# Kernel optimization log

Measured on AMD Instinct MI355X. Metric: run time of the kernel, lower is better.

The kernel has to match this reference:

```python
import jax, jax.numpy as jnp
import numpy as np

NH = 6
D = 78  # dim_k = dim_v, dk = dv = 13 per head
SCALE = 1.0 / np.sqrt(D // NH).astype(np.float32)


def _split(t):
    # (B, n, D) -> (B, H, n, dk)
    B, n, d = t.shape
    return t.reshape(B, n, NH, d // NH).transpose(0, 2, 1, 3)


def _merge(t):
    # (B, H, n, dk) -> (B, n, D)
    B, h, n, d = t.shape
    return t.transpose(0, 2, 1, 3).reshape(B, n, h * d)


def _cross_attn(x, y, Wq, Wk, Wv):
    # MultiHeadCrossSelfAttention / MultiHeadSelfAttention math (dropout=identity in eval;
    # attn_mask is expanded but never applied in the original forward).
    q = _split(x @ Wq)
    k = _split(y @ Wk)
    v = _split(y @ Wv)
    dist = jax.nn.softmax(jnp.einsum('bhqd,bhkd->bhqk', q, k) * SCALE, axis=-1)
    return _merge(jnp.einsum('bhqk,bhkd->bhqd', dist, v))


def _contrastive_attn(x, y, Wq, Wk, Wv):
    # MultiHeadContrastiveSelfAttention: softmax -> (1 - p) -> softmax -> matmul, residual q add.
    q = _split(x @ Wq)
    k = _split(y @ Wk)
    v = _split(y @ Wv)
    dist = jax.nn.softmax(jnp.einsum('bhqd,bhkd->bhqk', q, k) * SCALE, axis=-1)
    dist = jax.nn.softmax(1.0 - dist, axis=-1)
    return _merge(q + jnp.einsum('bhqk,bhkd->bhqd', dist, v))


def setup_inputs() -> dict:
    key = jax.random.key(0)
    ks = jax.random.split(key, 20)
    B, nT, nV, nA = 8, 1024, 1024, 1024
    inp = {
        'x': jax.random.normal(ks[0], (B, nT, D), jnp.float32),
        'y': jax.random.normal(ks[1], (B, nV, D), jnp.float32),
        'z': jax.random.normal(ks[2], (B, nA, D), jnp.float32),
        'mask_tv': jnp.zeros((B, nT, nV), jnp.bool_),
        'mask_ta': jnp.zeros((B, nT, nA), jnp.bool_),
    }
    names = ['Wq_tv', 'Wk_tv', 'Wv_tv', 'Wq_ta', 'Wk_ta', 'Wv_ta',
             'Wq_ctv', 'Wk_ctv', 'Wv_ctv', 'Wq_cta', 'Wk_cta', 'Wv_cta',
             'Wq_s', 'Wk_s', 'Wv_s']
    for i, nm in enumerate(names):
        inp[nm] = jax.random.normal(ks[3 + i], (D, D), jnp.float32) * 0.05
    return inp


def reference(x, y, z, mask_tv, mask_ta,
              Wq_tv, Wk_tv, Wv_tv, Wq_ta, Wk_ta, Wv_ta,
              Wq_ctv, Wk_ctv, Wv_ctv, Wq_cta, Wk_cta, Wv_cta,
              Wq_s, Wk_s, Wv_s):
    # masks are dead args in the original module (expanded but never applied)
    att_tv = _cross_attn(x, y, Wq_tv, Wk_tv, Wv_tv)          # MHSCA_TV
    att_ta = _cross_attn(x, z, Wq_ta, Wk_ta, Wv_ta)          # MHSCA_TA
    c_tv = _contrastive_attn(x, y, Wq_ctv, Wk_ctv, Wv_ctv)   # MHSCTA_TV
    c_ta = _contrastive_attn(x, z, Wq_cta, Wk_cta, Wv_cta)   # MHSCTA_TA
    # fuse three pooled modality tokens through the length-3 MHSA
    tokens = jnp.stack([x.mean(axis=1),
                        (att_tv + c_tv).mean(axis=1),
                        (att_ta + c_ta).mean(axis=1)], axis=1)  # (B, 3, D)
    fused = _cross_attn(tokens, tokens, Wq_s, Wk_s, Wv_s)       # MHSA
    # (B, 4*1024 + 3, D)
    return jnp.concatenate([att_tv, c_tv, att_ta, c_ta, fused], axis=1)
```

## Files before the change

kernel.cpp:

```cpp
#include <hip/hip_runtime.h>
#include <hip/hip_bf16.h>

#define BB 8
#define NN 1024
#define DM 78
#define NH 6
#define DK 13
#define NROW 4099
#define QSCL 0.40013158f
#define SCALE 0.27735009811261457f
#define INV1023 0.000977517106549365f

using bf16 = __hip_bfloat16;
typedef __attribute__((ext_vector_type(8))) short short8;
typedef __attribute__((ext_vector_type(4))) float f32x4;

#if __has_builtin(__builtin_amdgcn_exp2f)
#define EXP2(x) __builtin_amdgcn_exp2f(x)
#else
__device__ __forceinline__ float EXP2(float x) {
    float r;
    asm volatile("v_exp_f32 %0, %1\n\ts_nop 1" : "=v"(r) : "v"(x));
    return r;
}
#endif

#define MATSZ ((size_t)48 * 1024 * 16)

struct PW { const float* w[12]; };

__device__ __forceinline__ unsigned pkbf2(float a, float b) {
    __hip_bfloat162 t = __float22bfloat162_rn(make_float2(a, b));
    return *(unsigned*)&t;
}

union FRAG { unsigned u[4]; short8 s8; };

__global__ __launch_bounds__(256, 6) void proj_kernel(const float* __restrict__ x,
                                                      const float* __restrict__ y,
                                                      const float* __restrict__ z,
                                                      PW p,
                                                      unsigned* __restrict__ Qbf,
                                                      unsigned* __restrict__ Kbf,
                                                      unsigned* __restrict__ Vt,
                                                      float* __restrict__ Qf32,
                                                      float* __restrict__ sv,
                                                      float* __restrict__ tok) {
    __shared__ unsigned SMEM[6608];
    int bid = blockIdx.x;
    int tid = threadIdx.x;
    int mat, rb;
    if (bid < 256) { mat = 2 + (bid >> 7); rb = bid & 127; }
    else {
        int t = bid - 256;
        int midx = t >> 7;
        mat = (midx < 2) ? midx : midx + 2;
        rb = t & 127;
    }
    const float* src = (mat < 4) ? x : (((mat - 4) & 1) ? z : y);
    const float* sp = src + (size_t)rb * 64 * DM;
    const float* W = p.w[mat];
    int bb = rb >> 4;
    int i0 = (rb & 15) * 64;
    float* CT = (float*)SMEM;

    if (bid < 256) {
        float* AT = (float*)SMEM;
        float* WL = AT + 39 * 68;
        int rowg = tid >> 4, colg = tid & 15;
        float acc[4][5] = {{0.f}};
        for (int ch = 0; ch < 2; ++ch) {
            int e0 = ch * 39;
            if (ch) __syncthreads();
            for (int i = tid; i < 64 * 39; i += 256) {
                int r = i / 39, er = i - r * 39;
                AT[er * 68 + r] = sp[r * DM + e0 + er];
            }
            for (int i = tid; i < 39 * 80; i += 256) {
                int er = i / 80, c = i - er * 80;
                WL[er * 80 + c] = (c < DM) ? W[(size_t)(e0 + er) * DM + c] : 0.f;
            }
            __syncthreads();
            if (mat == 2 && tid < 39) {
                float s = 0.f;
                for (int r = 0; r < 64; ++r) s += AT[tid * 68 + r];
                atomicAdd(&tok[bb * DM + e0 + tid], s);
            }
            for (int er = 0; er < 39; ++er) {
                float4 a4 = *(const float4*)&AT[er * 68 + rowg * 4];
                float av[4] = {a4.x, a4.y, a4.z, a4.w};
                const float* wr = &WL[er * 80 + colg * 5];
                float w0 = wr[0], w1 = wr[1], w2 = wr[2], w3 = wr[3], w4 = wr[4];
#pragma unroll
                for (int j = 0; j < 4; ++j) {
                    acc[j][0] = fmaf(av[j], w0, acc[j][0]);
                    acc[j][1] = fmaf(av[j], w1, acc[j][1]);
                    acc[j][2] = fmaf(av[j], w2, acc[j][2]);
                    acc[j][3] = fmaf(av[j], w3, acc[j][3]);
                    acc[j][4] = fmaf(av[j], w4, acc[j][4]);
                }
            }
        }
        __syncthreads();
#pragma unroll
        for (int j = 0; j < 4; ++j)
#pragma unroll
            for (int k = 0; k < 5; ++k) {
                int c = colg * 5 + k;
                if (c < DM) CT[(rowg * 4 + j) * 81 + c] = acc[j][k];
            }
        __syncthreads();
        for (int t2 = tid; t2 < NH * 64 * 8; t2 += 256) {
            int hh = t2 >> 9;
            int rem = t2 & 511;
            int r = rem >> 3, cp = rem & 7;
            int c0 = cp * 2, c1 = cp * 2 + 1;
            float a = (c0 < DK) ? CT[r * 81 + hh * DK + c0] * QSCL : 0.f;
            float bv = (c1 < DK) ? CT[r * 81 + hh * DK + c1] * QSCL : 0.f;
            Qbf[(((size_t)mat * 48 + bb * NH + hh) * 1024 + i0 + r) * 8 + cp] = pkbf2(a, bv);
        }
        for (int t2 = tid; t2 < 64 * DM; t2 += 256) {
            int r = t2 / DM, c = t2 - r * DM;
            int hh = c / DK, dd = c - hh * DK;
            Qf32[((size_t)(mat - 2) * 48 + bb * NH + hh) * 1024 * DK +
                 (size_t)(i0 + r) * DK + dd] = CT[r * 81 + c];
        }
    } else {
        unsigned* ALu = SMEM;
        unsigned* WTu = SMEM + 64 * 52;
        const float2* sp2 = (const float2*)sp;
        for (int i = tid; i < 64 * 39; i += 256) {
            float2 f2 = sp2[i];
            int r = i / 39, pc = i - r * 39;
            ALu[r * 52 + pc] = pkbf2(f2.x, f2.y);
        }
        for (int i = tid; i < 64 * 13; i += 256) {
            int r = i / 13, pc = i - r * 13;
            ALu[r * 52 + 39 + pc] = 0u;
        }
        for (int i = tid; i < 41 * 80; i += 256) {
            int pc = i / 80, n = i - pc * 80;
            int k0 = pc * 2;
            float a = (n < DM && k0 < DM) ? W[(size_t)k0 * DM + n] : 0.f;
            float bv = (n < DM && k0 + 1 < DM) ? W[(size_t)(k0 + 1) * DM + n] : 0.f;
            WTu[n * 41 + pc] = pkbf2(a, bv);
        }
        __syncthreads();
        int wv = tid >> 6, lane = tid & 63, quad = lane >> 4, lq = lane & 15;
        int r0 = wv * 16;
        const short* ALs = (const short*)ALu;
        const short* WTs = (const short*)WTu;
        short8 af0 = *(const short8*)(ALs + (r0 + lq) * 104 + quad * 8);
        short8 af1 = *(const short8*)(ALs + (r0 + lq) * 104 + 32 + quad * 8);
        short8 af2 = *(const short8*)(ALs + (r0 + lq) * 104 + 64 + quad * 8);
        const f32x4 zz = {0.f, 0.f, 0.f, 0.f};
        f32x4 acc[5];
#pragma unroll
        for (int n = 0; n < 5; ++n) acc[n] = zz;
#pragma unroll
        for (int n = 0; n < 5; ++n) {
            const short* wb = WTs + (n * 16 + lq) * 82 + quad * 8;
            acc[n] = __builtin_amdgcn_mfma_f32_16x16x32_bf16(
                af0, *(const short8*)wb, acc[n], 0, 0, 0);
            acc[n] = __builtin_amdgcn_mfma_f32_16x16x32_bf16(
                af1, *(const short8*)(wb + 32), acc[n], 0, 0, 0);
            acc[n] = __builtin_amdgcn_mfma_f32_16x16x32_bf16(
                af2, *(const short8*)(wb + 64), acc[n], 0, 0, 0);
        }
        __syncthreads();
#pragma unroll
        for (int n = 0; n < 5; ++n) {
            int c = n * 16 + lq;
            if (c < DM) {
#pragma unroll
                for (int r = 0; r < 4; ++r)
                    CT[(r0 + quad * 4 + r) * 81 + c] = acc[n][r];
            }
        }
        __syncthreads();
        if (mat < 8) {
            unsigned* dst = (mat < 4) ? Qbf : Kbf;
            int m4 = (mat < 4) ? mat : mat - 4;
            float scl = (mat < 4) ? QSCL : 1.0f;
            for (int t2 = tid; t2 < NH * 64 * 8; t2 += 256) {
                int hh = t2 >> 9;
                int rem = t2 & 511;
                int r = rem >> 3, cp = rem & 7;
                int c0 = cp * 2, c1 = cp * 2 + 1;
                float a = (c0 < DK) ? CT[r * 81 + hh * DK + c0] * scl : 0.f;
                float bv = (c1 < DK) ? CT[r * 81 + hh * DK + c1] * scl : 0.f;
                dst[(((size_t)m4 * 48 + bb * NH + hh) * 1024 + i0 + r) * 8 + cp] = pkbf2(a, bv);
            }
        } else {
            for (int t2 = tid; t2 < NH * 16 * 32; t2 += 256) {
                int hh = t2 >> 9;
                int rem = t2 & 511;
                int dd = rem >> 5, cp = rem & 31;
                int pp = (cp & 15) * 2;
                int b2 = cp >> 4;
                int qd = pp >> 3, jj = pp & 7;
                int l0 = b2 * 32 + 4 * qd + (jj < 4 ? jj : 12 + jj);
                float a, bv;
                if (dd < DK) {
                    a = CT[l0 * 81 + hh * DK + dd];
                    bv = CT[(l0 + 1) * 81 + hh * DK + dd];
                } else if (dd == 13) { a = 1.f; bv = 1.f; }
                else { a = 0.f; bv = 0.f; }
                Vt[(((size_t)(mat - 8) * 48 + bb * NH + hh) * 16 + dd) * 512 +
                   (i0 >> 1) + cp] = pkbf2(a, bv);
            }
            if (mat >= 10 && tid < DM) {
                int hh = tid / DK, dd = tid - hh * DK;
                float s = 0.f;
                for (int r = 0; r < 64; ++r) s += CT[r * 81 + tid];
                atomicAdd(&sv[((size_t)(mat - 10) * 48 + bb * NH + hh) * DK + dd], s);
            }
        }
    }
}

__global__ __launch_bounds__(256) void att_kernel(const bf16* __restrict__ Qbf,
                                                  const bf16* __restrict__ Kbf,
                                                  const bf16* __restrict__ Vt,
                                                  const float* __restrict__ Qf32,
                                                  const float* __restrict__ sv,
                                                  float* __restrict__ tok,
                                                  float* __restrict__ out) {
    int bid = blockIdx.x;
    int qt = (bid >> 3) & 7;
    int ghb = (bid & 7) | ((bid >> 6) << 3);
    int h = ghb % NH;
    int r2 = ghb / NH;
    int b = r2 & 7;
    int g = r2 >> 3;
    int tid = threadIdx.x, wave = tid >> 6, lane = tid & 63;
    int quad = lane >> 4, lq = lane & 15;
    size_t mb = (size_t)g * 48 + b * NH + h;
    int q0 = qt * 64 + wave * 16;
    int q1 = q0 + 512;

    short8 zero8 = {0, 0, 0, 0, 0, 0, 0, 0};
    short8 qfA = zero8, qfB = zero8;
    if (quad < 2) {
        qfA = *(const short8*)((const short*)Qbf + (mb * 1024 + q0 + lq) * 16 + quad * 8);
        qfB = *(const short8*)((const short*)Qbf + (mb * 1024 + q1 + lq) * 16 + quad * 8);
    }
    const short* Kp = (const short*)Kbf + mb * 1024 * 16;
    const short* Vp = (const short*)Vt + mb * 16 * 1024 + (size_t)lq * 1024;
    f32x4 OA = {0.f, 0.f, 0.f, 0.f};
    f32x4 OB = {0.f, 0.f, 0.f, 0.f};
    const f32x4 zz = {0.f, 0.f, 0.f, 0.f};

    short8 kX0 = zero8, kX1 = zero8, kY0 = zero8, kY1 = zero8, vX, vY;
    if (quad < 2) {
        kX0 = *(const short8*)(Kp + lq * 16 + quad * 8);
        kX1 = *(const short8*)(Kp + (16 + lq) * 16 + quad * 8);
        kY0 = *(const short8*)(Kp + (32 + lq) * 16 + quad * 8);
        kY1 = *(const short8*)(Kp + (48 + lq) * 16 + quad * 8);
    }
    vX = *(const short8*)(Vp + quad * 8);
    vY = *(const short8*)(Vp + 32 + quad * 8);

    for (int kt = 0; kt < 16; ++kt) {
        int nkey = kt * 64 + 64;
        f32x4 SX0 = __builtin_amdgcn_mfma_f32_16x16x32_bf16(kX0, qfA, zz, 0, 0, 0);
        f32x4 SX1 = __builtin_amdgcn_mfma_f32_16x16x32_bf16(kX1, qfA, zz, 0, 0, 0);
        f32x4 SX2 = __builtin_amdgcn_mfma_f32_16x16x32_bf16(kX0, qfB, zz, 0, 0, 0);
        f32x4 SX3 = __builtin_amdgcn_mfma_f32_16x16x32_bf16(kX1, qfB, zz, 0, 0, 0);
        f32x4 SY0 = __builtin_amdgcn_mfma_f32_16x16x32_bf16(kY0, qfA, zz, 0, 0, 0);
        f32x4 SY1 = __builtin_amdgcn_mfma_f32_16x16x32_bf16(kY1, qfA, zz, 0, 0, 0);
        f32x4 SY2 = __builtin_amdgcn_mfma_f32_16x16x32_bf16(kY0, qfB, zz, 0, 0, 0);
        f32x4 SY3 = __builtin_amdgcn_mfma_f32_16x16x32_bf16(kY1, qfB, zz, 0, 0, 0);
        short8 kX0n = zero8, kX1n = zero8, kY0n = zero8, kY1n = zero8, vXn, vYn;
        if (quad < 2) {
            kX0n = *(const short8*)(Kp + (nkey + lq) * 16 + quad * 8);
            kX1n = *(const short8*)(Kp + (nkey + 16 + lq) * 16 + quad * 8);
            kY0n = *(const short8*)(Kp + (nkey + 32 + lq) * 16 + quad * 8);
            kY1n = *(const short8*)(Kp + (nkey + 48 + lq) * 16 + quad * 8);
        }
        vXn = *(const short8*)(Vp + nkey + quad * 8);
        vYn = *(const short8*)(Vp + nkey + 32 + quad * 8);

        FRAG aXA, aXB, aYA, aYB;
        aXA.u[0] = pkbf2(EXP2(SX0[0]), EXP2(SX0[1]));
        aXA.u[1] = pkbf2(EXP2(SX0[2]), EXP2(SX0[3]));
        aXA.u[2] = pkbf2(EXP2(SX1[0]), EXP2(SX1[1]));
        aXA.u[3] = pkbf2(EXP2(SX1[2]), EXP2(SX1[3]));
        OA = __builtin_amdgcn_mfma_f32_16x16x32_bf16(aXA.s8, vX, OA, 0, 0, 0);
        aXB.u[0] = pkbf2(EXP2(SX2[0]), EXP2(SX2[1]));
        aXB.u[1] = pkbf2(EXP2(SX2[2]), EXP2(SX2[3]));
        aXB.u[2] = pkbf2(EXP2(SX3[0]), EXP2(SX3[1]));
        aXB.u[3] = pkbf2(EXP2(SX3[2]), EXP2(SX3[3]));
        OB = __builtin_amdgcn_mfma_f32_16x16x32_bf16(aXB.s8, vX, OB, 0, 0, 0);
        aYA.u[0] = pkbf2(EXP2(SY0[0]), EXP2(SY0[1]));
        aYA.u[1] = pkbf2(EXP2(SY0[2]), EXP2(SY0[3]));
        aYA.u[2] = pkbf2(EXP2(SY1[0]), EXP2(SY1[1]));
        aYA.u[3] = pkbf2(EXP2(SY1[2]), EXP2(SY1[3]));
        OA = __builtin_amdgcn_mfma_f32_16x16x32_bf16(aYA.s8, vY, OA, 0, 0, 0);
        aYB.u[0] = pkbf2(EXP2(SY2[0]), EXP2(SY2[1]));
        aYB.u[1] = pkbf2(EXP2(SY2[2]), EXP2(SY2[3]));
        aYB.u[2] = pkbf2(EXP2(SY3[0]), EXP2(SY3[1]));
        aYB.u[3] = pkbf2(EXP2(SY3[2]), EXP2(SY3[3]));
        OB = __builtin_amdgcn_mfma_f32_16x16x32_bf16(aYB.s8, vY, OB, 0, 0, 0);
        kX0 = kX0n; kX1 = kX1n; kY0 = kY0n; kY1 = kY1n; vX = vXn; vY = vYn;
    }

    size_t rowbase = (g == 0) ? 0 : (g == 1 ? 2 * NN : (g == 2 ? NN : 3 * NN));
    float lA[4], lB[4];
#pragma unroll
    for (int r = 0; r < 4; ++r) {
        lA[r] = __shfl(OA[r], (lane & 48) | 13, 64);
        lB[r] = __shfl(OB[r], (lane & 48) | 13, 64);
    }
    float svv = 0.f;
    const float* qf32p = nullptr;
    if (g >= 2) {
        if (lq < DK) svv = sv[((size_t)(g - 2) * 48 + b * NH + h) * DK + lq];
        qf32p = Qf32 + ((size_t)(g - 2) * 48 + b * NH + h) * 1024 * DK + lq;
    }
    float vsum = 0.f;
#pragma unroll
    for (int r = 0; r < 4; ++r) {
        int mA = q0 + quad * 4 + r;
        int mB = q1 + quad * 4 + r;
        float A0 = OA[r] / lA[r];
        float A1 = OB[r] / lB[r];
        float v0, v1;
        if (g < 2) { v0 = A0; v1 = A1; }
        else {
            float qr0 = (lq < DK) ? qf32p[(size_t)mA * DK] : 0.f;
            float qr1 = (lq < DK) ? qf32p[(size_t)mB * DK] : 0.f;
            v0 = qr0 + (svv - A0) * INV1023;
            v1 = qr1 + (svv - A1) * INV1023;
        }
        if (lq < DK) {
            out[((size_t)b * NROW + rowbase + mA) * DM + h * DK + lq] = v0;
            out[((size_t)b * NROW + rowbase + mB) * DM + h * DK + lq] = v1;
            vsum += v0 + v1;
        }
    }
    vsum += __shfl_xor(vsum, 16);
    vsum += __shfl_xor(vsum, 32);
    if (quad == 0 && lq < DK) {
        int tki = (g & 1) ? 2 : 1;
        atomicAdd(&tok[(size_t)tki * (8 * DM) + b * DM + h * DK + lq], vsum);
    }
}

__global__ __launch_bounds__(256) void fused_kernel(const float* __restrict__ tok,
                                                    const float* __restrict__ Wq,
                                                    const float* __restrict__ Wk,
                                                    const float* __restrict__ Wv,
                                                    float* __restrict__ out) {
    __shared__ float T[3 * DM], Qs[3 * DM], Ks[3 * DM], Vs[3 * DM], P[NH * 9];
    int b = blockIdx.x, tid = threadIdx.x;
    if (tid < 234) {
        int t = tid / DM, d = tid - t * DM;
        T[tid] = tok[(size_t)t * (8 * DM) + b * DM + d] * (1.f / NN);
    }
    __syncthreads();
    for (int idx = tid; idx < 702; idx += 256) {
        int mat = idx / 234;
        int rem = idx - mat * 234;
        int t = rem / DM, d = rem - t * DM;
        const float* W = (mat == 0) ? Wq : (mat == 1 ? Wk : Wv);
        float a = 0.f;
        for (int e = 0; e < DM; ++e) a = fmaf(T[t * DM + e], W[(size_t)e * DM + d], a);
        float* dst = (mat == 0) ? Qs : (mat == 1 ? Ks : Vs);
        dst[t * DM + d] = a;
    }
    __syncthreads();
    if (tid < NH * 3) {
        int h = tid / 3, t = tid % 3;
        float s[3];
        for (int k = 0; k < 3; ++k) {
            float a = 0.f;
            for (int d2 = 0; d2 < DK; ++d2)
                a += Qs[t * DM + h * DK + d2] * Ks[k * DM + h * DK + d2];
            s[k] = a * SCALE;
        }
        float mm = fmaxf(s[0], fmaxf(s[1], s[2]));
        float e0 = __expf(s[0] - mm), e1 = __expf(s[1] - mm), e2 = __expf(s[2] - mm);
        float inv = 1.f / (e0 + e1 + e2);
        P[(h * 3 + t) * 3 + 0] = e0 * inv;
        P[(h * 3 + t) * 3 + 1] = e1 * inv;
        P[(h * 3 + t) * 3 + 2] = e2 * inv;
    }
    __syncthreads();
    if (tid < 234) {
        int t = tid / DM, d = tid - t * DM, h = d / DK;
        float a = 0.f;
        for (int k = 0; k < 3; ++k) a += P[(h * 3 + t) * 3 + k] * Vs[k * DM + d];
        out[((size_t)b * NROW + 4 * NN + t) * DM + d] = a;
    }
}

extern "C" void kernel_launch(void* const* d_in, const int* in_sizes, int n_in,
                              void* d_out, int out_size, void* d_ws, size_t ws_size,
                              hipStream_t stream) {
    const float* bigs[3] = {nullptr, nullptr, nullptr};
    const float* w[15];
    int nb = 0, nw = 0;
    for (int i = 0; i < n_in; ++i) {
        if (in_sizes[i] == BB * NN * DM && nb < 3) bigs[nb++] = (const float*)d_in[i];
        else if (in_sizes[i] == DM * DM && nw < 15) w[nw++] = (const float*)d_in[i];
    }
    if (nb < 3 || nw < 15) {
        bigs[0] = (const float*)d_in[0]; bigs[1] = (const float*)d_in[1];
        bigs[2] = (const float*)d_in[2];
        int base = (n_in >= 20) ? 5 : 3;
        for (int i = 0; i < 15; ++i) w[i] = (const float*)d_in[base + i];
    }
    const float* x = bigs[0];
    const float* y = bigs[1];
    const float* z = bigs[2];
    float* out = (float*)d_out;

    bf16* Qbf = (bf16*)d_ws;
    bf16* Kbf = Qbf + 4 * MATSZ;
    bf16* Vt  = Kbf + 4 * MATSZ;
    float* Qf32 = (float*)(Vt + 4 * MATSZ);
    float* sv = Qf32 + (size_t)2 * 48 * 1024 * DK;
    float* tok = sv + 2 * 48 * DK;

    PW pp;
    const float* wsel[12] = {w[0], w[3], w[6], w[9],
                             w[1], w[4], w[7], w[10],
                             w[2], w[5], w[8], w[11]};
    for (int i = 0; i < 12; ++i) pp.w[i] = wsel[i];

    hipMemsetAsync(sv, 0, (2 * 48 * DK + 3 * 8 * DM) * sizeof(float), stream);
    proj_kernel<<<1536, 256, 0, stream>>>(x, y, z, pp, (unsigned*)Qbf, (unsigned*)Kbf,
                                          (unsigned*)Vt, Qf32, sv, tok);
    att_kernel<<<4 * BB * NH * 8, 256, 0, stream>>>(Qbf, Kbf, Vt, Qf32, sv, tok, out);
    fused_kernel<<<BB, 256, 0, stream>>>(tok, w[12], w[13], w[14], out);
}
```

Measured before the change: 212.5 us.

## Unify projection onto MFMA path and use K=16 MFMA with deeper prefetch in attention

The projection kernel drops its scalar-FMA fp32 path for the x-based Q matrices and runs all matrices through the bf16 MFMA path, computing token sums from the bf16-packed tile. The attention loop replaces the zero-padded 16x16x32 score MFMAs with 16x16x16 MFMAs on 4-element K/Q fragments, which halves wasted score work. It also double-buffers K/V fragments two tiles ahead, unrolls the loop, and raises wave priority around the score MFMAs. In exchange, Qf32 and the token mean now come from bf16-rounded inputs, which costs accuracy, and the prefetch reads past the last tile and uses more registers.

```diff
diff --git a/kernel.cpp b/kernel.cpp
--- a/kernel.cpp
+++ b/kernel.cpp
@@ -13,6 +13,7 @@
 
 using bf16 = __hip_bfloat16;
 typedef __attribute__((ext_vector_type(8))) short short8;
+typedef __attribute__((ext_vector_type(4))) short short4v;
 typedef __attribute__((ext_vector_type(4))) float f32x4;
 
 #if __has_builtin(__builtin_amdgcn_exp2f)
@@ -24,6 +25,8 @@
     return r;
 }
 #endif
+
+#define SMFMA(k, q, c) __builtin_amdgcn_mfma_f32_16x16x16bf16_1k((k), (q), (c), 0, 0, 0)
 
 #define MATSZ ((size_t)48 * 1024 * 16)
 
@@ -49,14 +52,8 @@
     __shared__ unsigned SMEM[6608];
     int bid = blockIdx.x;
     int tid = threadIdx.x;
-    int mat, rb;
-    if (bid < 256) { mat = 2 + (bid >> 7); rb = bid & 127; }
-    else {
-        int t = bid - 256;
-        int midx = t >> 7;
-        mat = (midx < 2) ? midx : midx + 2;
-        rb = t & 127;
-    }
+    int mat = bid >> 7;
+    int rb = bid & 127;
     const float* src = (mat < 4) ? x : (((mat - 4) & 1) ? z : y);
     const float* sp = src + (size_t)rb * 64 * DM;
     const float* W = p.w[mat];
@@ -64,157 +61,113 @@
     int i0 = (rb & 15) * 64;
     float* CT = (float*)SMEM;
 
-    if (bid < 256) {
-        float* AT = (float*)SMEM;
-        float* WL = AT + 39 * 68;
-        int rowg = tid >> 4, colg = tid & 15;
-        float acc[4][5] = {{0.f}};
-        for (int ch = 0; ch < 2; ++ch) {
-            int e0 = ch * 39;
-            if (ch) __syncthreads();
-            for (int i = tid; i < 64 * 39; i += 256) {
-                int r = i / 39, er = i - r * 39;
-                AT[er * 68 + r] = sp[r * DM + e0 + er];
-            }
-            for (int i = tid; i < 39 * 80; i += 256) {
-                int er = i / 80, c = i - er * 80;
-                WL[er * 80 + c] = (c < DM) ? W[(size_t)(e0 + er) * DM + c] : 0.f;
-            }
-            __syncthreads();
-            if (mat == 2 && tid < 39) {
-                float s = 0.f;
-                for (int r = 0; r < 64; ++r) s += AT[tid * 68 + r];
-                atomicAdd(&tok[bb * DM + e0 + tid], s);
-            }
-            for (int er = 0; er < 39; ++er) {
-                float4 a4 = *(const float4*)&AT[er * 68 + rowg * 4];
-                float av[4] = {a4.x, a4.y, a4.z, a4.w};
-                const float* wr = &WL[er * 80 + colg * 5];
-                float w0 = wr[0], w1 = wr[1], w2 = wr[2], w3 = wr[3], w4 = wr[4];
-#pragma unroll
-                for (int j = 0; j < 4; ++j) {
-                    acc[j][0] = fmaf(av[j], w0, acc[j][0]);
-                    acc[j][1] = fmaf(av[j], w1, acc[j][1]);
-                    acc[j][2] = fmaf(av[j], w2, acc[j][2]);
-                    acc[j][3] = fmaf(av[j], w3, acc[j][3]);
-                    acc[j][4] = fmaf(av[j], w4, acc[j][4]);
-                }
-            }
-        }
-        __syncthreads();
-#pragma unroll
-        for (int j = 0; j < 4; ++j)
-#pragma unroll
-            for (int k = 0; k < 5; ++k) {
-                int c = colg * 5 + k;
-                if (c < DM) CT[(rowg * 4 + j) * 81 + c] = acc[j][k];
-            }
-        __syncthreads();
+    unsigned* ALu = SMEM;
+    unsigned* WTu = SMEM + 64 * 52;
+    const float2* sp2 = (const float2*)sp;
+    for (int i = tid; i < 64 * 39; i += 256) {
+        float2 f2 = sp2[i];
+        int r = i / 39, pc = i - r * 39;
+        ALu[r * 52 + pc] = pkbf2(f2.x, f2.y);
+    }
+    for (int i = tid; i < 64 * 13; i += 256) {
+        int r = i / 13, pc = i - r * 13;
+        ALu[r * 52 + 39 + pc] = 0u;
+    }
+    for (int i = tid; i < 41 * 80; i += 256) {
+        int pc = i / 80, n = i - pc * 80;
+        int k0 = pc * 2;
+        float a = (n < DM && k0 < DM) ? W[(size_t)k0 * DM + n] : 0.f;
+        float bv = (n < DM && k0 + 1 < DM) ? W[(size_t)(k0 + 1) * DM + n] : 0.f;
+        WTu[n * 41 + pc] = pkbf2(a, bv);
+    }
+    __syncthreads();
+    if (mat == 0 && tid < 39) {
+        const unsigned* col = ALu + tid;
+        float s0 = 0.f, s1 = 0.f;
+        for (int r = 0; r < 64; ++r) {
+            unsigned u = col[r * 52];
+            s0 += __uint_as_float(u << 16);
+            s1 += __uint_as_float(u & 0xffff0000u);
+        }
+        atomicAdd(&tok[bb * DM + tid * 2], s0);
+        atomicAdd(&tok[bb * DM + tid * 2 + 1], s1);
+    }
+    int wv = tid >> 6, lane = tid & 63, quad = lane >> 4, lq = lane & 15;
+    int r0 = wv * 16;
+    const short* ALs = (const short*)ALu;
+    const short* WTs = (const short*)WTu;
+    short8 af0 = *(const short8*)(ALs + (r0 + lq) * 104 + quad * 8);
+    short8 af1 = *(const short8*)(ALs + (r0 + lq) * 104 + 32 + quad * 8);
+    short8 af2 = *(const short8*)(ALs + (r0 + lq) * 104 + 64 + quad * 8);
+    const f32x4 zz = {0.f, 0.f, 0.f, 0.f};
+    f32x4 acc[5];
+#pragma unroll
+    for (int n = 0; n < 5; ++n) acc[n] = zz;
+#pragma unroll
+    for (int n = 0; n < 5; ++n) {
+        const short* wb = WTs + (n * 16 + lq) * 82 + quad * 8;
+        acc[n] = __builtin_amdgcn_mfma_f32_16x16x32_bf16(
+            af0, *(const short8*)wb, acc[n], 0, 0, 0);
+        acc[n] = __builtin_amdgcn_mfma_f32_16x16x32_bf16(
+            af1, *(const short8*)(wb + 32), acc[n], 0, 0, 0);
+        acc[n] = __builtin_amdgcn_mfma_f32_16x16x32_bf16(
+            af2, *(const short8*)(wb + 64), acc[n], 0, 0, 0);
+    }
+    __syncthreads();
+#pragma unroll
+    for (int n = 0; n < 5; ++n) {
+        int c = n * 16 + lq;
+        if (c < DM) {
+#pragma unroll
+            for (int r = 0; r < 4; ++r)
+                CT[(r0 + quad * 4 + r) * 81 + c] = acc[n][r];
+        }
+    }
+    __syncthreads();
+    if (mat < 8) {
+        unsigned* dst = (mat < 4) ? Qbf : Kbf;
+        int m4 = (mat < 4) ? mat : mat - 4;
+        float scl = (mat < 4) ? QSCL : 1.0f;
         for (int t2 = tid; t2 < NH * 64 * 8; t2 += 256) {
             int hh = t2 >> 9;
             int rem = t2 & 511;
             int r = rem >> 3, cp = rem & 7;
             int c0 = cp * 2, c1 = cp * 2 + 1;
-            float a = (c0 < DK) ? CT[r * 81 + hh * DK + c0] * QSCL : 0.f;
-            float bv = (c1 < DK) ? CT[r * 81 + hh * DK + c1] * QSCL : 0.f;
-            Qbf[(((size_t)mat * 48 + bb * NH + hh) * 1024 + i0 + r) * 8 + cp] = pkbf2(a, bv);
-        }
-        for (int t2 = tid; t2 < 64 * DM; t2 += 256) {
-            int r = t2 / DM, c = t2 - r * DM;
-            int hh = c / DK, dd = c - hh * DK;
-            Qf32[((size_t)(mat - 2) * 48 + bb * NH + hh) * 1024 * DK +
-                 (size_t)(i0 + r) * DK + dd] = CT[r * 81 + c];
+            float a = (c0 < DK) ? CT[r * 81 + hh * DK + c0] * scl : 0.f;
+            float bv = (c1 < DK) ? CT[r * 81 + hh * DK + c1] * scl : 0.f;
+            dst[(((size_t)m4 * 48 + bb * NH + hh) * 1024 + i0 + r) * 8 + cp] = pkbf2(a, bv);
+        }
+        if (mat >= 2 && mat < 4) {
+            for (int t2 = tid; t2 < 64 * DM; t2 += 256) {
+                int r = t2 / DM, c = t2 - r * DM;
+                int hh = c / DK, dd = c - hh * DK;
+                Qf32[((size_t)(mat - 2) * 48 + bb * NH + hh) * 1024 * DK +
+                     (size_t)(i0 + r) * DK + dd] = CT[r * 81 + c];
+            }
         }
     } else {
-        unsigned* ALu = SMEM;
-        unsigned* WTu = SMEM + 64 * 52;
-        const float2* sp2 = (const float2*)sp;
-        for (int i = tid; i < 64 * 39; i += 256) {
-            float2 f2 = sp2[i];
-            int r = i / 39, pc = i - r * 39;
-            ALu[r * 52 + pc] = pkbf2(f2.x, f2.y);
-        }
-        for (int i = tid; i < 64 * 13; i += 256) {
-            int r = i / 13, pc = i - r * 13;
-            ALu[r * 52 + 39 + pc] = 0u;
-        }
-        for (int i = tid; i < 41 * 80; i += 256) {
-            int pc = i / 80, n = i - pc * 80;
-            int k0 = pc * 2;
-            float a = (n < DM && k0 < DM) ? W[(size_t)k0 * DM + n] : 0.f;
-            float bv = (n < DM && k0 + 1 < DM) ? W[(size_t)(k0 + 1) * DM + n] : 0.f;
-            WTu[n * 41 + pc] = pkbf2(a, bv);
-        }
-        __syncthreads();
-        int wv = tid >> 6, lane = tid & 63, quad = lane >> 4, lq = lane & 15;
-        int r0 = wv * 16;
-        const short* ALs = (const short*)ALu;
-        const short* WTs = (const short*)WTu;
-        short8 af0 = *(const short8*)(ALs + (r0 + lq) * 104 + quad * 8);
-        short8 af1 = *(const short8*)(ALs + (r0 + lq) * 104 + 32 + quad * 8);
-        short8 af2 = *(const short8*)(ALs + (r0 + lq) * 104 + 64 + quad * 8);
-        const f32x4 zz = {0.f, 0.f, 0.f, 0.f};
-        f32x4 acc[5];
-#pragma unroll
-        for (int n = 0; n < 5; ++n) acc[n] = zz;
-#pragma unroll
-        for (int n = 0; n < 5; ++n) {
-            const short* wb = WTs + (n * 16 + lq) * 82 + quad * 8;
-            acc[n] = __builtin_amdgcn_mfma_f32_16x16x32_bf16(
-                af0, *(const short8*)wb, acc[n], 0, 0, 0);
-            acc[n] = __builtin_amdgcn_mfma_f32_16x16x32_bf16(
-                af1, *(const short8*)(wb + 32), acc[n], 0, 0, 0);
-            acc[n] = __builtin_amdgcn_mfma_f32_16x16x32_bf16(
-                af2, *(const short8*)(wb + 64), acc[n], 0, 0, 0);
-        }
-        __syncthreads();
-#pragma unroll
-        for (int n = 0; n < 5; ++n) {
-            int c = n * 16 + lq;
-            if (c < DM) {
-#pragma unroll
-                for (int r = 0; r < 4; ++r)
-                    CT[(r0 + quad * 4 + r) * 81 + c] = acc[n][r];
-            }
-        }
-        __syncthreads();
-        if (mat < 8) {
-            unsigned* dst = (mat < 4) ? Qbf : Kbf;
-            int m4 = (mat < 4) ? mat : mat - 4;
-            float scl = (mat < 4) ? QSCL : 1.0f;
-            for (int t2 = tid; t2 < NH * 64 * 8; t2 += 256) {
-                int hh = t2 >> 9;
-                int rem = t2 & 511;
-                int r = rem >> 3, cp = rem & 7;
-                int c0 = cp * 2, c1 = cp * 2 + 1;
-                float a = (c0 < DK) ? CT[r * 81 + hh * DK + c0] * scl : 0.f;
-                float bv = (c1 < DK) ? CT[r * 81 + hh * DK + c1] * scl : 0.f;
-                dst[(((size_t)m4 * 48 + bb * NH + hh) * 1024 + i0 + r) * 8 + cp] = pkbf2(a, bv);
-            }
-        } else {
-            for (int t2 = tid; t2 < NH * 16 * 32; t2 += 256) {
-                int hh = t2 >> 9;
-                int rem = t2 & 511;
-                int dd = rem >> 5, cp = rem & 31;
-                int pp = (cp & 15) * 2;
-                int b2 = cp >> 4;
-                int qd = pp >> 3, jj = pp & 7;
-                int l0 = b2 * 32 + 4 * qd + (jj < 4 ? jj : 12 + jj);
-                float a, bv;
-                if (dd < DK) {
-                    a = CT[l0 * 81 + hh * DK + dd];
-                    bv = CT[(l0 + 1) * 81 + hh * DK + dd];
-                } else if (dd == 13) { a = 1.f; bv = 1.f; }
-                else { a = 0.f; bv = 0.f; }
-                Vt[(((size_t)(mat - 8) * 48 + bb * NH + hh) * 16 + dd) * 512 +
-                   (i0 >> 1) + cp] = pkbf2(a, bv);
-            }
-            if (mat >= 10 && tid < DM) {
-                int hh = tid / DK, dd = tid - hh * DK;
-                float s = 0.f;
-                for (int r = 0; r < 64; ++r) s += CT[r * 81 + tid];
-                atomicAdd(&sv[((size_t)(mat - 10) * 48 + bb * NH + hh) * DK + dd], s);
-            }
+        for (int t2 = tid; t2 < NH * 16 * 32; t2 += 256) {
+            int hh = t2 >> 9;
+            int rem = t2 & 511;
+            int dd = rem >> 5, cp = rem & 31;
+            int pp = (cp & 15) * 2;
+            int b2 = cp >> 4;
+            int qd = pp >> 3, jj = pp & 7;
+            int l0 = b2 * 32 + 4 * qd + (jj < 4 ? jj : 12 + jj);
+            float a, bv;
+            if (dd < DK) {
+                a = CT[l0 * 81 + hh * DK + dd];
+                bv = CT[(l0 + 1) * 81 + hh * DK + dd];
+            } else if (dd == 13) { a = 1.f; bv = 1.f; }
+            else { a = 0.f; bv = 0.f; }
+            Vt[(((size_t)(mat - 8) * 48 + bb * NH + hh) * 16 + dd) * 512 +
+               (i0 >> 1) + cp] = pkbf2(a, bv);
+        }
+        if (mat >= 10 && tid < DM) {
+            int hh = tid / DK, dd = tid - hh * DK;
+            float s = 0.f;
+            for (int r = 0; r < 64; ++r) s += CT[r * 81 + tid];
+            atomicAdd(&sv[((size_t)(mat - 10) * 48 + bb * NH + hh) * DK + dd], s);
         }
     }
 }
@@ -239,70 +192,75 @@
     int q0 = qt * 64 + wave * 16;
     int q1 = q0 + 512;
 
-    short8 zero8 = {0, 0, 0, 0, 0, 0, 0, 0};
-    short8 qfA = zero8, qfB = zero8;
-    if (quad < 2) {
-        qfA = *(const short8*)((const short*)Qbf + (mb * 1024 + q0 + lq) * 16 + quad * 8);
-        qfB = *(const short8*)((const short*)Qbf + (mb * 1024 + q1 + lq) * 16 + quad * 8);
-    }
     const short* Kp = (const short*)Kbf + mb * 1024 * 16;
     const short* Vp = (const short*)Vt + mb * 16 * 1024 + (size_t)lq * 1024;
     f32x4 OA = {0.f, 0.f, 0.f, 0.f};
     f32x4 OB = {0.f, 0.f, 0.f, 0.f};
     const f32x4 zz = {0.f, 0.f, 0.f, 0.f};
 
-    short8 kX0 = zero8, kX1 = zero8, kY0 = zero8, kY1 = zero8, vX, vY;
-    if (quad < 2) {
-        kX0 = *(const short8*)(Kp + lq * 16 + quad * 8);
-        kX1 = *(const short8*)(Kp + (16 + lq) * 16 + quad * 8);
-        kY0 = *(const short8*)(Kp + (32 + lq) * 16 + quad * 8);
-        kY1 = *(const short8*)(Kp + (48 + lq) * 16 + quad * 8);
-    }
-    vX = *(const short8*)(Vp + quad * 8);
-    vY = *(const short8*)(Vp + 32 + quad * 8);
-
+    short4v qfA = *(const short4v*)((const short*)Qbf + (mb * 1024 + q0 + lq) * 16 + quad * 4);
+    short4v qfB = *(const short4v*)((const short*)Qbf + (mb * 1024 + q1 + lq) * 16 + quad * 4);
+    int ko = quad * 4;
+
+    short4v kX0a = *(const short4v*)(Kp + lq * 16 + ko);
+    short4v kX1a = *(const short4v*)(Kp + 256 + lq * 16 + ko);
+    short4v kY0a = *(const short4v*)(Kp + 512 + lq * 16 + ko);
+    short4v kY1a = *(const short4v*)(Kp + 768 + lq * 16 + ko);
+    short8 vXa = *(const short8*)(Vp + quad * 8);
+    short8 vYa = *(const short8*)(Vp + 32 + quad * 8);
+    short4v kX0b = *(const short4v*)(Kp + 1024 + lq * 16 + ko);
+    short4v kX1b = *(const short4v*)(Kp + 1280 + lq * 16 + ko);
+    short4v kY0b = *(const short4v*)(Kp + 1536 + lq * 16 + ko);
+    short4v kY1b = *(const short4v*)(Kp + 1792 + lq * 16 + ko);
+    short8 vXb = *(const short8*)(Vp + 64 + quad * 8);
+    short8 vYb = *(const short8*)(Vp + 96 + quad * 8);
+
+    const short* Kit = Kp + 2048;
+    const short* Vit = Vp + 128;
+
+#pragma unroll
     for (int kt = 0; kt < 16; ++kt) {
-        int nkey = kt * 64 + 64;
-        f32x4 SX0 = __builtin_amdgcn_mfma_f32_16x16x32_bf16(kX0, qfA, zz, 0, 0, 0);
-        f32x4 SX1 = __builtin_amdgcn_mfma_f32_16x16x32_bf16(kX1, qfA, zz, 0, 0, 0);
-        f32x4 SX2 = __builtin_amdgcn_mfma_f32_16x16x32_bf16(kX0, qfB, zz, 0, 0, 0);
-        f32x4 SX3 = __builtin_amdgcn_mfma_f32_16x16x32_bf16(kX1, qfB, zz, 0, 0, 0);
-        f32x4 SY0 = __builtin_amdgcn_mfma_f32_16x16x32_bf16(kY0, qfA, zz, 0, 0, 0);
-        f32x4 SY1 = __builtin_amdgcn_mfma_f32_16x16x32_bf16(kY1, qfA, zz, 0, 0, 0);
-        f32x4 SY2 = __builtin_amdgcn_mfma_f32_16x16x32_bf16(kY0, qfB, zz, 0, 0, 0);
-        f32x4 SY3 = __builtin_amdgcn_mfma_f32_16x16x32_bf16(kY1, qfB, zz, 0, 0, 0);
-        short8 kX0n = zero8, kX1n = zero8, kY0n = zero8, kY1n = zero8, vXn, vYn;
-        if (quad < 2) {
-            kX0n = *(const short8*)(Kp + (nkey + lq) * 16 + quad * 8);
-            kX1n = *(const short8*)(Kp + (nkey + 16 + lq) * 16 + quad * 8);
-            kY0n = *(const short8*)(Kp + (nkey + 32 + lq) * 16 + quad * 8);
-            kY1n = *(const short8*)(Kp + (nkey + 48 + lq) * 16 + quad * 8);
-        }
-        vXn = *(const short8*)(Vp + nkey + quad * 8);
-        vYn = *(const short8*)(Vp + nkey + 32 + quad * 8);
+        __builtin_amdgcn_s_setprio(1);
+        f32x4 SX0 = SMFMA(kX0a, qfA, zz);
+        f32x4 SX1 = SMFMA(kX1a, qfA, zz);
+        f32x4 SX2 = SMFMA(kX0a, qfB, zz);
+        f32x4 SX3 = SMFMA(kX1a, qfB, zz);
+        f32x4 SY0 = SMFMA(kY0a, qfA, zz);
+        f32x4 SY1 = SMFMA(kY1a, qfA, zz);
+        f32x4 SY2 = SMFMA(kY0a, qfB, zz);
+        f32x4 SY3 = SMFMA(kY1a, qfB, zz);
+        __builtin_amdgcn_s_setprio(0);
+        short4v kX0n = *(const short4v*)(Kit + lq * 16 + ko);
+        short4v kX1n = *(const short4v*)(Kit + 256 + lq * 16 + ko);
+        short4v kY0n = *(const short4v*)(Kit + 512 + lq * 16 + ko);
+        short4v kY1n = *(const short4v*)(Kit + 768 + lq * 16 + ko);
+        short8 vXn = *(const short8*)(Vit + quad * 8);
+        short8 vYn = *(const short8*)(Vit + 32 + quad * 8);
+        Kit += 1024; Vit += 64;
 
         FRAG aXA, aXB, aYA, aYB;
         aXA.u[0] = pkbf2(EXP2(SX0[0]), EXP2(SX0[1]));
         aXA.u[1] = pkbf2(EXP2(SX0[2]), EXP2(SX0[3]));
         aXA.u[2] = pkbf2(EXP2(SX1[0]), EXP2(SX1[1]));
         aXA.u[3] = pkbf2(EXP2(SX1[2]), EXP2(SX1[3]));
-        OA = __builtin_amdgcn_mfma_f32_16x16x32_bf16(aXA.s8, vX, OA, 0, 0, 0);
+        OA = __builtin_amdgcn_mfma_f32_16x16x32_bf16(aXA.s8, vXa, OA, 0, 0, 0);
         aXB.u[0] = pkbf2(EXP2(SX2[0]), EXP2(SX2[1]));
         aXB.u[1] = pkbf2(EXP2(SX2[2]), EXP2(SX2[3]));
         aXB.u[2] = pkbf2(EXP2(SX3[0]), EXP2(SX3[1]));
         aXB.u[3] = pkbf2(EXP2(SX3[2]), EXP2(SX3[3]));
-        OB = __builtin_amdgcn_mfma_f32_16x16x32_bf16(aXB.s8, vX, OB, 0, 0, 0);
+        OB = __builtin_amdgcn_mfma_f32_16x16x32_bf16(aXB.s8, vXa, OB, 0, 0, 0);
         aYA.u[0] = pkbf2(EXP2(SY0[0]), EXP2(SY0[1]));
         aYA.u[1] = pkbf2(EXP2(SY0[2]), EXP2(SY0[3]));
         aYA.u[2] = pkbf2(EXP2(SY1[0]), EXP2(SY1[1]));
         aYA.u[3] = pkbf2(EXP2(SY1[2]), EXP2(SY1[3]));
-        OA = __builtin_amdgcn_mfma_f32_16x16x32_bf16(aYA.s8, vY, OA, 0, 0, 0);
+        OA = __builtin_amdgcn_mfma_f32_16x16x32_bf16(aYA.s8, vYa, OA, 0, 0, 0);
         aYB.u[0] = pkbf2(EXP2(SY2[0]), EXP2(SY2[1]));
         aYB.u[1] = pkbf2(EXP2(SY2[2]), EXP2(SY2[3]));
         aYB.u[2] = pkbf2(EXP2(SY3[0]), EXP2(SY3[1]));
         aYB.u[3] = pkbf2(EXP2(SY3[2]), EXP2(SY3[3]));
-        OB = __builtin_amdgcn_mfma_f32_16x16x32_bf16(aYB.s8, vY, OB, 0, 0, 0);
-        kX0 = kX0n; kX1 = kX1n; kY0 = kY0n; kY1 = kY1n; vX = vXn; vY = vYn;
+        OB = __builtin_amdgcn_mfma_f32_16x16x32_bf16(aYB.s8, vYa, OB, 0, 0, 0);
+        kX0a = kX0b; kX1a = kX1b; kY0a = kY0b; kY1a = kY1b; vXa = vXb; vYa = vYb;
+        kX0b = kX0n; kX1b = kX1n; kY0b = kY0n; kY1b = kY1n; vXb = vXn; vYb = vYn;
     }
 
     size_t rowbase = (g == 0) ? 0 : (g == 1 ? 2 * NN : (g == 2 ? NN : 3 * NN));
```

Result: no change. 208.9 us (-1.7%).
